# Kernel optimization log

Measured on AMD Instinct MI355X. Metric: run time of the kernel, lower is better.

The kernel has to match this reference:

```python
import jax, jax.numpy as jnp
import numpy as np
from jax import lax

ALPHA = 100.0      # SuperSpike surrogate slope (LIFParameters alpha)
DT = 1e-3          # norse default dt
TAU_SYN_INV = 200.0
TAU_MEM_INV = 100.0
V_TH = 1.0

@jax.custom_vjp
def superspike(x):
    return (x > 0).astype(x.dtype)

def _ss_fwd(x):
    return (x > 0).astype(x.dtype), x

def _ss_bwd(x, g):
    return (g / (ALPHA * jnp.abs(x) + 1.0) ** 2,)

superspike.defvjp(_ss_fwd, _ss_bwd)

def lif_step(inp, v, i):
    # norse lif_step: decay v/i, spike on v_decayed - v_th, reset, then add input current
    v_dec = v + DT * TAU_MEM_INV * (-v + i)
    i_dec = i * (1.0 - DT * TAU_SYN_INV)
    z = superspike(v_dec - V_TH)
    v_new = (1.0 - z) * v_dec  # v_reset = 0
    i_new = i_dec + inp
    return z, v_new, i_new

def li_step(inp, v, i):
    # leaky integrator readout (LILinearCell): returns membrane voltage
    v_new = v + DT * TAU_MEM_INV * (-v + i)
    i_new = i * (1.0 - DT * TAU_SYN_INV) + inp
    return v_new, v_new, i_new

def conv2d(x, w, b):
    y = lax.conv_general_dilated(x, w, (1, 1), 'VALID',
                                 dimension_numbers=('NCHW', 'OIHW', 'NCHW'))
    return y + b[None, :, None, None]

def maxpool2(x):
    return lax.reduce_window(x, -jnp.inf, lax.max, (1, 1, 2, 2), (1, 1, 2, 2), 'VALID')

def setup_inputs() -> dict:
    key = jax.random.key(0)
    ks = jax.random.split(key, 9)
    T, B, C, H = 16, 64, 3, 64
    feats = int(((H - 4) / 2 - 4) / 2)  # 13
    def unif(k, shape, fan_in):
        bound = 1.0 / np.sqrt(fan_in)
        return jax.random.uniform(k, shape, jnp.float32, -bound, bound)
    return {
        'x':  jax.random.normal(ks[0], (T, B, C, H, H), jnp.float32),
        'w1': unif(ks[1], (32, C, 5, 5), C * 25),
        'b1': unif(ks[2], (32,), C * 25),
        'w2': unif(ks[3], (64, 32, 5, 5), 32 * 25),
        'b2': unif(ks[4], (64,), 32 * 25),
        'wf': unif(ks[5], (1024, feats * feats * 64), feats * feats * 64),
        'bf': unif(ks[6], (1024,), feats * feats * 64),
        'wo': unif(ks[7], (10, 1024), 1024),
        'bo': unif(ks[8], (10,), 1024),
    }

def reference(x, w1, b1, w2, b2, wf, bf, wo, bo):
    T, B, C, H, _ = x.shape
    h1 = H - 4           # conv1 out spatial
    p1 = h1 // 2         # pool1
    h2 = p1 - 4          # conv2 out spatial
    p2 = h2 // 2         # pool2 (== features)
    dtype = x.dtype
    zeros = lambda s: jnp.zeros(s, dtype)
    carry0 = (zeros((B, 32, h1, h1)), zeros((B, 32, h1, h1)),   # lif0 v, i
              zeros((B, 64, h2, h2)), zeros((B, 64, h2, h2)),   # lif1 v, i
              zeros((B, 1024)), zeros((B, 1024)),               # lif2 v, i
              zeros((B, 10)), zeros((B, 10)))                   # out  v, i

    def step(carry, xt):
        v0, i0, v1, i1, v2, i2, vo, io = carry
        z = conv2d(xt, w1, b1)
        z, v0, i0 = lif_step(z, v0, i0)
        z = maxpool2(z)
        z = 10.0 * conv2d(z, w2, b2)
        z, v1, i1 = lif_step(z, v1, i1)
        z = maxpool2(z)
        z = z.reshape(B, -1)
        z = z @ wf.T + bf
        z, v2, i2 = lif_step(z, v2, i2)
        inp = jax.nn.relu(z) @ wo.T + bo
        v, vo, io = li_step(inp, vo, io)
        return (v0, i0, v1, i1, v2, i2, vo, io), v

    _, voltages = lax.scan(step, carry0, x)
    return voltages  # [T, B, 10]
```

## Files before the change

### kernel.cpp

```cpp
#include <hip/hip_runtime.h>

typedef __attribute__((ext_vector_type(8))) short short8v;
typedef __attribute__((ext_vector_type(4))) float f32x4;

#define DT_TM 0.1f
#define SYN_DEC 0.8f
#define TT 16
#define BB 64
#define FCK 10816

#define BO_S1   ((size_t)0)
#define BO_S2   ((size_t)29491200)
#define BO_S3   ((size_t)51642368)
#define BO_PART ((size_t)55836672)
#define BO_WH2  BO_PART
#define BO_WL2  (BO_PART + 102400)
#define BO_AFW  (BO_PART + 204800)
#define BO_WHF  ((size_t)72613888)
#define BO_WLF  ((size_t)94765056)
#define BIG_NEED ((size_t)116916224)

#define FO_S1   ((size_t)0)
#define FO_S2   ((size_t)29491200)
#define FO_S3   ((size_t)40566784)
#define FO_PART ((size_t)44761088)
#define FO_V2   ((size_t)51576832)
#define FO_I2   ((size_t)51838976)
#define FO_WH2  FO_PART
#define FO_WL2  (FO_PART + 102400)

__device__ __forceinline__ unsigned short bf16_rne(float f) {
  unsigned int u = __float_as_uint(f);
  return (unsigned short)((u + 0x7FFFu + ((u >> 16) & 1u)) >> 16);
}

__global__ __launch_bounds__(256) void k0_prep(
    const float* __restrict__ w2, unsigned short* __restrict__ whi,
    unsigned short* __restrict__ wlo) {
  int e = blockIdx.x * 256 + threadIdx.x;
  if (e >= 25 * 64 * 32) return;
  int kk = e >> 11;
  int rem = e & 2047;
  int oc = rem >> 5, c = rem & 31;
  float w = w2[(size_t)(oc * 32 + c) * 25 + kk];
  unsigned short hi = bf16_rne(w);
  float fhi = __uint_as_float((unsigned int)hi << 16);
  unsigned short lo = bf16_rne(w - fhi);
  whi[e] = hi;
  wlo[e] = lo;
}

__global__ __launch_bounds__(256) void k0b_wf(
    const float* __restrict__ wf, unsigned short* __restrict__ whiF,
    unsigned short* __restrict__ wloF) {
  size_t e = (size_t)blockIdx.x * 256 + threadIdx.x;
  if (e >= (size_t)1024 * FCK) return;
  float w = wf[e];
  unsigned short hi = bf16_rne(w);
  float fhi = __uint_as_float((unsigned int)hi << 16);
  whiF[e] = hi;
  wloF[e] = bf16_rne(w - fhi);
}

__global__ __launch_bounds__(256) void k0w_prep(
    const float* __restrict__ w1, unsigned short* __restrict__ afw) {
  int e = blockIdx.x * 256 + threadIdx.x;
  if (e >= 9216) return;
  int i = e & 7, l = (e >> 3) & 63, f = e >> 9;
  int sp = f % 3, ks = (f / 3) % 3, mt = f / 9;
  int oc = mt * 16 + (l & 15);
  int tap = (l >> 4) * 8 + i;
  unsigned short out = 0;
  int ky = tap / 6, kx = tap - 6 * ky;
  if (tap < 30 && kx < 5) {
    float v = w1[(oc * 3 + ks) * 25 + ky * 5 + kx];
    unsigned short h = bf16_rne(v);
    if (sp == 0) out = h;
    else {
      float r1 = v - __uint_as_float((unsigned int)h << 16);
      unsigned short m = bf16_rne(r1);
      if (sp == 1) out = m;
      else out = bf16_rne(r1 - __uint_as_float((unsigned int)m << 16));
    }
  }
  afw[e] = out;
}

#define MFMA_BF16 __builtin_amdgcn_mfma_f32_16x16x32_bf16

__global__ __launch_bounds__(256) void k1_mfma(
    const float* __restrict__ x, const unsigned short* __restrict__ afw,
    const float* __restrict__ b1, unsigned char* __restrict__ s1) {
  __shared__ unsigned int Hp[2][18 * 81];
  __shared__ unsigned int Mp[2][18 * 81];
  __shared__ unsigned int Lp[2][18 * 81];
  const int s = blockIdx.x;
  const int b = blockIdx.y;
  const int tid = threadIdx.x;
  const int w = tid >> 6, l = tid & 63;
  const int n = l & 15, tg = l >> 4;
  const int xpix = 16 * w + n;
  const int xcl = (xpix < 60) ? xpix : 59;
  const bool storer = ((n & 1) == 0) && (xpix < 60);

  short8v aw[2][3][3];
#pragma unroll
  for (int mt = 0; mt < 2; ++mt)
#pragma unroll
    for (int ks = 0; ks < 3; ++ks)
#pragma unroll
      for (int sp = 0; sp < 3; ++sp)
        aw[mt][ks][sp] =
            *(const short8v*)(afw + (((mt * 3 + ks) * 3 + sp) * 64 + l) * 8);

  f32x4 bias0 = *(const f32x4*)&b1[tg * 4];
  f32x4 bias1 = *(const f32x4*)&b1[16 + tg * 4];

  int poff[4];
#pragma unroll
  for (int i = 0; i < 4; ++i) {
    int tap = tg * 8 + 2 * i;
    int ky = tap / 6, kx = tap - 6 * ky;
    if (tap >= 30) { ky = 4; kx = 0; }
    poff[i] = ky * 81 + kx;
  }

  const int jrow0 = tid >> 5, jcp0 = tid & 31;
  const int jrow1 = (tid + 256) >> 5, jcp1 = jcp0;
  const int jrow2 = (tid + 512) >> 5, jcp2 = jcp0;
  const bool job2 = tid < 64;
  const int slan = (l & 32) | ((l + 1) & 31);

  float vst[2][2][4], ist[2][2][4];
#pragma unroll
  for (int a = 0; a < 2; ++a)
#pragma unroll
    for (int m = 0; m < 2; ++m)
#pragma unroll
      for (int r = 0; r < 4; ++r) { vst[a][m][r] = 0.f; ist[a][m][r] = 0.f; }

  float2 pf0, pf1, pf2;

  auto phaseA = [&](int t) {
    const float* xp = x + ((size_t)(t * BB + b)) * 12288 + (size_t)(2 * s) * 64;
    {
      int c = jrow0 / 6, r = jrow0 - 6 * c;
      pf0 = *(const float2*)(xp + c * 4096 + r * 64 + 2 * jcp0);
    }
    {
      int c = jrow1 / 6, r = jrow1 - 6 * c;
      pf1 = *(const float2*)(xp + c * 4096 + r * 64 + 2 * jcp1);
    }
    if (job2) {
      int c = jrow2 / 6, r = jrow2 - 6 * c;
      pf2 = *(const float2*)(xp + c * 4096 + r * 64 + 2 * jcp2);
    }
  };

  auto phaseB = [&](int bfi) {
    unsigned int* H = Hp[bfi];
    unsigned int* M = Mp[bfi];
    unsigned int* L = Lp[bfi];
#pragma unroll
    for (int j = 0; j < 3; ++j) {
      if (j == 2 && !job2) break;
      float2 v2 = (j == 0) ? pf0 : (j == 1) ? pf1 : pf2;
      int row = (j == 0) ? jrow0 : (j == 1) ? jrow1 : jrow2;
      int cp = jcp0;
      unsigned int h0 = bf16_rne(v2.x);
      float r0 = v2.x - __uint_as_float(h0 << 16);
      unsigned int m0 = bf16_rne(r0);
      unsigned int l0 = bf16_rne(r0 - __uint_as_float(m0 << 16));
      unsigned int h1 = bf16_rne(v2.y);
      float r1 = v2.y - __uint_as_float(h1 << 16);
      unsigned int m1 = bf16_rne(r1);
      unsigned int l1 = bf16_rne(r1 - __uint_as_float(m1 << 16));
      unsigned int hm0 = h0 | (m0 << 16);
      unsigned int hmN = (unsigned int)__shfl((int)hm0, slan);
      unsigned int lN  = (unsigned int)__shfl((int)l0, slan);
      int d = row * 81 + 2 * cp;
      H[d]     = h0 | (h1 << 16);
      H[d + 1] = h1 | (hmN << 16);
      M[d]     = m0 | (m1 << 16);
      M[d + 1] = m1 | (hmN & 0xffff0000u);
      L[d]     = l0 | (l1 << 16);
      L[d + 1] = l1 | (lN << 16);
    }
  };

  phaseA(0);
  phaseB(0);
  __syncthreads();

  for (int t = 0; t < TT; ++t) {
    const int cur = t & 1;
    if (t + 1 < TT) phaseA(t + 1);

    const unsigned int* H = Hp[cur];
    const unsigned int* M = Mp[cur];
    const unsigned int* L = Lp[cur];

    unsigned int pk[2];
#pragma unroll
    for (int nt = 0; nt < 2; ++nt) {
      f32x4 acc0 = (f32x4){0.f, 0.f, 0.f, 0.f};
      f32x4 acc1 = (f32x4){0.f, 0.f, 0.f, 0.f};
#pragma unroll
      for (int ks = 0; ks < 3; ++ks) {
        const int base = (ks * 6 + nt) * 81 + xcl;
        union { unsigned int u[4]; short8v v; } fH, fM, fL;
#pragma unroll
        for (int i = 0; i < 4; ++i) {
          fH.u[i] = H[base + poff[i]];
          fM.u[i] = M[base + poff[i]];
          fL.u[i] = L[base + poff[i]];
        }
        acc0 = MFMA_BF16(aw[0][ks][2], fH.v, acc0, 0, 0, 0);
        acc1 = MFMA_BF16(aw[1][ks][2], fH.v, acc1, 0, 0, 0);
        acc0 = MFMA_BF16(aw[0][ks][1], fM.v, acc0, 0, 0, 0);
        acc1 = MFMA_BF16(aw[1][ks][1], fM.v, acc1, 0, 0, 0);
        acc0 = MFMA_BF16(aw[0][ks][0], fL.v, acc0, 0, 0, 0);
        acc1 = MFMA_BF16(aw[1][ks][0], fL.v, acc1, 0, 0, 0);
        acc0 = MFMA_BF16(aw[0][ks][1], fH.v, acc0, 0, 0, 0);
        acc1 = MFMA_BF16(aw[1][ks][1], fH.v, acc1, 0, 0, 0);
        acc0 = MFMA_BF16(aw[0][ks][0], fM.v, acc0, 0, 0, 0);
        acc1 = MFMA_BF16(aw[1][ks][0], fM.v, acc1, 0, 0, 0);
        acc0 = MFMA_BF16(aw[0][ks][0], fH.v, acc0, 0, 0, 0);
        acc1 = MFMA_BF16(aw[1][ks][0], fH.v, acc1, 0, 0, 0);
      }
      unsigned int nib0 = 0, nib1 = 0;
#pragma unroll
      for (int r = 0; r < 4; ++r) {
        float inp = acc0[r] + bias0[r];
        float vd = vst[nt][0][r] + DT_TM * (ist[nt][0][r] - vst[nt][0][r]);
        float id = SYN_DEC * ist[nt][0][r];
        bool z = vd > 1.0f;
        vst[nt][0][r] = z ? 0.f : vd;
        ist[nt][0][r] = id + inp;
// ... 37 lines not shown
  const int tid = threadIdx.x;
  const bool valid = tid < 225;
  const int py0 = (tid / 15) * 2;
  const int px0 = (tid % 15) * 2;
  const int br = 2 * py0;
  const int bc = 2 * px0;

  float v[16], cur[16];
#pragma unroll
  for (int j = 0; j < 16; ++j) { v[j] = 0.f; cur[j] = 0.f; }
  const float bias = b1[oc];

  for (int t = 0; t < TT; ++t) {
    const float* xp = x + ((size_t)(t * BB + b)) * 12288;
#pragma unroll
    for (int k = 0; k < 12; ++k) {
      int e = tid + k * 256;
      int row = e >> 4, c4 = e & 15;
      ((float4*)xs)[row * 17 + c4] = ((const float4*)xp)[e];
    }
    __syncthreads();

    if (valid) {
      float acc[4][4];
#pragma unroll
      for (int r = 0; r < 4; ++r)
#pragma unroll
        for (int s = 0; s < 4; ++s) acc[r][s] = 0.f;

#pragma unroll
      for (int c = 0; c < 3; ++c) {
        const float* wp = w1 + (oc * 3 + c) * 25;
        float wv[25];
#pragma unroll
        for (int j = 0; j < 25; ++j) wv[j] = wp[j];
#pragma unroll
        for (int ri = 0; ri < 8; ++ri) {
          const float* rowp = &xs[(c * 64 + br + ri) * 68 + bc];
          float4 ra = *(const float4*)rowp;
          float4 rb = *(const float4*)(rowp + 4);
          float row[8] = {ra.x, ra.y, ra.z, ra.w, rb.x, rb.y, rb.z, rb.w};
#pragma unroll
          for (int r = 0; r < 4; ++r) {
            int ky = ri - r;
            if (ky >= 0 && ky < 5) {
#pragma unroll
              for (int kx = 0; kx < 5; ++kx) {
                float w = wv[ky * 5 + kx];
#pragma unroll
                for (int s = 0; s < 4; ++s) acc[r][s] += w * row[s + kx];
              }
            }
          }
        }
      }

      unsigned char pz00 = 0, pz01 = 0, pz10 = 0, pz11 = 0;
#pragma unroll
      for (int r = 0; r < 4; ++r)
#pragma unroll
        for (int s = 0; s < 4; ++s) {
          int j = r * 4 + s;
          float vd = v[j] + DT_TM * (cur[j] - v[j]);
          float id = SYN_DEC * cur[j];
          float inp = acc[r][s] + bias;
          bool z = vd > 1.0f;
          v[j] = z ? 0.f : vd;
          cur[j] = id + inp;
          if (z) {
            if (r < 2) { if (s < 2) pz00 = 1; else pz01 = 1; }
            else       { if (s < 2) pz10 = 1; else pz11 = 1; }
          }
        }
      size_t pixb = ((size_t)(t * BB + b)) * 900;
      s1[(pixb + (size_t)py0 * 30 + px0) * 32 + oc]           = pz00;
      s1[(pixb + (size_t)py0 * 30 + px0 + 1) * 32 + oc]       = pz01;
      s1[(pixb + (size_t)(py0 + 1) * 30 + px0) * 32 + oc]     = pz10;
      s1[(pixb + (size_t)(py0 + 1) * 30 + px0 + 1) * 32 + oc] = pz11;
    }
    __syncthreads();
  }
}

template<int NT>
__device__ __forceinline__ void k2_wave(
    const unsigned short* sl, float* Vst, float* Ist, unsigned char* zbuf,
    const unsigned short* __restrict__ whi, const unsigned short* __restrict__ wlo,
    const float* __restrict__ b2, int og, int q, int n, int ntstart, int npos) {
  int baddr[NT], pcl[NT];
  f32x4 acc[2][NT];
#pragma unroll
  for (int j = 0; j < NT; ++j) {
    int pl = (ntstart + j) * 16 + n;
    if (pl > npos - 1) pl = npos - 1;
    pcl[j] = pl;
    int ry = pl / 26, xx = pl - ry * 26;
    baddr[j] = (ry * 30 + xx) * 32 + q * 8;
    acc[0][j] = (f32x4){0.f, 0.f, 0.f, 0.f};
    acc[1][j] = (f32x4){0.f, 0.f, 0.f, 0.f};
  }
  const int abase = (og * 32 + n) * 32 + q * 8;
#pragma unroll 5
  for (int kk = 0; kk < 25; ++kk) {
    const int ky = kk / 5, kx = kk - (kk / 5) * 5;
    const int off = (ky * 30 + kx) * 32;
    short8v ah0 = *(const short8v*)(whi + kk * 2048 + abase);
    short8v al0 = *(const short8v*)(wlo + kk * 2048 + abase);
    short8v ah1 = *(const short8v*)(whi + kk * 2048 + abase + 512);
    short8v al1 = *(const short8v*)(wlo + kk * 2048 + abase + 512);
#pragma unroll
    for (int j = 0; j < NT; ++j) {
      short8v bv = *(const short8v*)(sl + baddr[j] + off);
      acc[0][j] = MFMA_BF16(al0, bv, acc[0][j], 0, 0, 0);
      acc[0][j] = MFMA_BF16(ah0, bv, acc[0][j], 0, 0, 0);
      acc[1][j] = MFMA_BF16(al1, bv, acc[1][j], 0, 0, 0);
      acc[1][j] = MFMA_BF16(ah1, bv, acc[1][j], 0, 0, 0);
    }
  }
  const f32x4 bias0 = *(const f32x4*)&b2[og * 32 + q * 4];
  const f32x4 bias1 = *(const f32x4*)&b2[og * 32 + 16 + q * 4];
#pragma unroll
  for (int j = 0; j < NT; ++j) {
    int p = pcl[j];
#pragma unroll
    for (int mi = 0; mi < 2; ++mi) {
      int sidx = p * 68 + og * 32 + mi * 16 + q * 4;
      f32x4 v4 = *(f32x4*)&Vst[sidx];
      f32x4 i4 = *(f32x4*)&Ist[sidx];
      f32x4 bia = mi ? bias1 : bias0;
      f32x4 a = acc[mi][j];
      unsigned char zr[4];
#pragma unroll
      for (int r = 0; r < 4; ++r) {
        float vd = v4[r] + DT_TM * (i4[r] - v4[r]);
        float id = SYN_DEC * i4[r];
        float inp = 10.f * (a[r] + bia[r]);
        bool z = vd > 1.0f;
        v4[r] = z ? 0.f : vd;
        i4[r] = id + inp;
        zr[r] = z ? 1 : 0;
      }
      *(f32x4*)&Vst[sidx] = v4;
      *(f32x4*)&Ist[sidx] = i4;
      *(uchar4*)&zbuf[sidx] = make_uchar4(zr[0], zr[1], zr[2], zr[3]);
    }
  }
}

template<typename ST>
__global__ __launch_bounds__(256) void k2_mfma(
    const unsigned char* __restrict__ s1, const unsigned short* __restrict__ whi,
    const unsigned short* __restrict__ wlo, const float* __restrict__ b2,
    ST* __restrict__ s2) {
  __shared__ unsigned short sl[12 * 30 * 32];
  __shared__ float Vst[208 * 68];
  __shared__ float Ist[208 * 68];
  __shared__ unsigned char zbuf[208 * 68];
  const int quad = blockIdx.x, b = blockIdx.y;
  const int tid = threadIdx.x;
  const int wid = tid >> 6, l = tid & 63;
  const int og = wid & 1, nc = wid >> 1;
  const int q = l >> 4, n = l & 15;
  const int y0 = (quad == 0) ? 0 : (2 + quad * 6);
  const int R  = (quad == 0) ? 8 : 6;
  const int inRows = R + 4;
  const int npos = R * 26;

  for (int e = tid; e < 208 * 68; e += 256) { Vst[e] = 0.f; Ist[e] = 0.f; }
  __syncthreads();

  for (int t = 0; t < TT; ++t) {
    const unsigned char* sp =
        s1 + (((size_t)(t * BB + b)) * 900 + (size_t)y0 * 30) * 32;
    const int nelem = inRows * 240;
    for (int e = tid; e < nelem; e += 256) {
      unsigned int w = *(const unsigned int*)(sp + (size_t)e * 4);
      unsigned int lo = ((w & 0xFFu) ? 0x3F80u : 0u) |
                        ((w & 0xFF00u) ? 0x3F800000u : 0u);
      unsigned int hi = ((w & 0xFF0000u) ? 0x3F80u : 0u) |
                        ((w & 0xFF000000u) ? 0x3F800000u : 0u);
      ((unsigned int*)sl)[e * 2]     = lo;
      ((unsigned int*)sl)[e * 2 + 1] = hi;
    }
    __syncthreads();

    if (quad == 0) {
      if (nc == 0) k2_wave<7>(sl, Vst, Ist, zbuf, whi, wlo, b2, og, q, n, 0, npos);
      else         k2_wave<6>(sl, Vst, Ist, zbuf, whi, wlo, b2, og, q, n, 7, npos);
    } else {
      k2_wave<5>(sl, Vst, Ist, zbuf, whi, wlo, b2, og, q, n, nc * 5, npos);
    }
    __syncthreads();

    const int pr = R >> 1;
    const int pcount = pr * 13 * 64;
    ST* s2p = s2 + ((size_t)(t * BB + b)) * 64 * 169;
    const int gpy0 = y0 >> 1;
    const ST one = (ST)((sizeof(ST) == 2) ? 0x3F80 : 1);
    for (int e = tid; e < pcount; e += 256) {
      int oc = e & 63, pp = e >> 6;
      int ppy = pp / 13, ppx = pp - ppy * 13;
      int base = (2 * ppy * 26 + 2 * ppx) * 68 + oc;
      unsigned char z = (unsigned char)(zbuf[base] | zbuf[base + 68] |
                        zbuf[base + 26 * 68] | zbuf[base + 26 * 68 + 68]);
      s2p[(size_t)oc * 169 + (gpy0 + ppy) * 13 + ppx] = z ? one : (ST)0;
    }
    __syncthreads();
  }
}

__global__ __launch_bounds__(512) void k3g_fc(
    const unsigned short* __restrict__ s2,
    const unsigned short* __restrict__ whiF,
    const unsigned short* __restrict__ wloF,
    float* __restrict__ part) {
  __shared__ __align__(16) unsigned short As[128][72];
  __shared__ __align__(16) unsigned short Bh[128][72];
  __shared__ __align__(16) unsigned short Bl[128][72];
  const int tid = threadIdx.x;
  const int w = tid >> 6, l = tid & 63;
  const int mh = w & 1, nq = w >> 1;
  const int lr = l & 15, lk = l >> 4;
  const int n0 = blockIdx.x * 128, m0 = blockIdx.y * 128;
  const int ks = blockIdx.z;
  const int s_begin = (169 * ks) >> 2, s_end = (169 * (ks + 1)) >> 2;

  const int arow = tid >> 2, aseg = tid & 3;
  const unsigned short* ap = s2 + (size_t)(m0 + arow) * FCK + aseg * 16;
  unsigned short* aq = &As[0][0] + arow * 72 + aseg * 16;
  const int barr = tid >> 8, brem = tid & 255;
  const int bn = brem >> 1, bhalf = brem & 1;
  const unsigned short* bp =
      (barr ? wloF : whiF) + (size_t)(n0 + bn) * FCK + bhalf * 32;
  unsigned short* bq = (barr ? &Bl[0][0] : &Bh[0][0]) + bn * 72 + bhalf * 32;

  f32x4 acc[4][2];
#pragma unroll
  for (int mt = 0; mt < 4; ++mt)
#pragma unroll
    for (int nt = 0; nt < 2; ++nt) acc[mt][nt] = (f32x4){0.f, 0.f, 0.f, 0.f};

  for (int s = s_begin; s < s_end; ++s) {
    const size_t k0 = (size_t)s * 64;
    short8v a0 = *(const short8v*)(ap + k0);
    short8v a1 = *(const short8v*)(ap + k0 + 8);
    short8v b0 = *(const short8v*)(bp + k0);
    short8v b1 = *(const short8v*)(bp + k0 + 8);
    short8v b2v = *(const short8v*)(bp + k0 + 16);
    short8v b3 = *(const short8v*)(bp + k0 + 24);
    __syncthreads();
    *(short8v*)(aq)      = a0;
    *(short8v*)(aq + 8)  = a1;
    *(short8v*)(bq)      = b0;
    *(short8v*)(bq + 8)  = b1;
    *(short8v*)(bq + 16) = b2v;
    *(short8v*)(bq + 24) = b3;
    __syncthreads();
#pragma unroll
    for (int kt = 0; kt < 2; ++kt) {
      short8v bh0 = *(const short8v*)&Bh[nq * 32 + lr][kt * 32 + lk * 8];
      short8v bh1 = *(const short8v*)&Bh[nq * 32 + 16 + lr][kt * 32 + lk * 8];
      short8v bl0 = *(const short8v*)&Bl[nq * 32 + lr][kt * 32 + lk * 8];
      short8v bl1 = *(const short8v*)&Bl[nq * 32 + 16 + lr][kt * 32 + lk * 8];
#pragma unroll
      for (int mt = 0; mt < 4; ++mt) {
        short8v af = *(const short8v*)&As[mh * 64 + mt * 16 + lr][kt * 32 + lk * 8];
        acc[mt][0] = MFMA_BF16(af, bh0, acc[mt][0], 0, 0, 0);
        acc[mt][0] = MFMA_BF16(af, bl0, acc[mt][0], 0, 0, 0);
        acc[mt][1] = MFMA_BF16(af, bh1, acc[mt][1], 0, 0, 0);
        acc[mt][1] = MFMA_BF16(af, bl1, acc[mt][1], 0, 0, 0);
      }
    }
  }
  float* pp = part + ((size_t)ks << 20);
#pragma unroll
  for (int mt = 0; mt < 4; ++mt)
#pragma unroll
    for (int nt = 0; nt < 2; ++nt) {
      int mrow = m0 + mh * 64 + mt * 16 + lk * 4;
      int ncol = n0 + nq * 32 + nt * 16 + lr;
#pragma unroll
      for (int r = 0; r < 4; ++r)
        pp[(size_t)(mrow + r) * 1024 + ncol] = acc[mt][nt][r];
    }
}

__global__ __launch_bounds__(256) void k3r_lif2(
    const float* __restrict__ part, const float* __restrict__ bf,
    float* __restrict__ s3) {
  int e = blockIdx.x * 256 + threadIdx.x;
// ... 57 lines not shown
      float a0 = av.x, a1 = av.y, a2 = av.z, a3 = av.w;
      acc[0][0] += a0 * bv.x; acc[0][1] += a0 * bv.y; acc[0][2] += a0 * bv.z; acc[0][3] += a0 * bv.w;
      acc[1][0] += a1 * bv.x; acc[1][1] += a1 * bv.y; acc[1][2] += a1 * bv.z; acc[1][3] += a1 * bv.w;
      acc[2][0] += a2 * bv.x; acc[2][1] += a2 * bv.y; acc[2][2] += a2 * bv.z; acc[2][3] += a2 * bv.w;
      acc[3][0] += a3 * bv.x; acc[3][1] += a3 * bv.y; acc[3][2] += a3 * bv.z; acc[3][3] += a3 * bv.w;
    }
  }
#pragma unroll
  for (int i = 0; i < 4; ++i)
#pragma unroll
    for (int j = 0; j < 4; ++j)
      part[((size_t)(ks * 64 + m0 + i)) * 1024 + N0 + n0 + j] = acc[i][j];
}

__global__ __launch_bounds__(256) void k3b_lif2(
    const float* __restrict__ part, const float* __restrict__ bf,
    float* __restrict__ v2, float* __restrict__ i2,
    float* __restrict__ s3, int t) {
  int e = blockIdx.x * 256 + threadIdx.x;
  int n = e & 1023;
  float s = 0.f;
#pragma unroll
  for (int ks = 0; ks < 26; ++ks) s += part[(size_t)ks * 65536 + e];
  float z = s + bf[n];
  float vv = v2[e], ii = i2[e];
  float vd = vv + DT_TM * (ii - vv);
  float id = SYN_DEC * ii;
  bool sp = vd > 1.0f;
  v2[e] = sp ? 0.f : vd;
  i2[e] = id + z;
  s3[(size_t)t * 65536 + e] = sp ? 1.f : 0.f;
}

__global__ __launch_bounds__(320) void k4_out(
    const float* __restrict__ s3, const float* __restrict__ wo,
    const float* __restrict__ bo, float* __restrict__ out) {
  const int b = blockIdx.x;
  const int g = threadIdx.x >> 5;
  const int l = threadIdx.x & 31;
  float vv = 0.f, ii = 0.f;
  const float bg = bo[g];
  for (int t = 0; t < TT; ++t) {
    const float* zp = s3 + ((size_t)t * BB + b) * 1024;
    const float* wp = wo + g * 1024;
    float p = 0.f;
#pragma unroll 8
    for (int j = l; j < 1024; j += 32) p += zp[j] * wp[j];
#pragma unroll
    for (int off = 16; off; off >>= 1) p += __shfl_down(p, off, 32);
    float inp = p + bg;
    float vn = vv + DT_TM * (ii - vv);
    if (l == 0) out[(size_t)(t * BB + b) * 10 + g] = vn;
    ii = SYN_DEC * ii + inp;
    vv = vn;
  }
}

extern "C" void kernel_launch(void* const* d_in, const int* in_sizes, int n_in,
                              void* d_out, int out_size, void* d_ws, size_t ws_size,
                              hipStream_t stream) {
  (void)in_sizes; (void)n_in; (void)out_size;
  const float* x  = (const float*)d_in[0];
  const float* w1 = (const float*)d_in[1];
  const float* b1 = (const float*)d_in[2];
  const float* w2 = (const float*)d_in[3];
  const float* b2 = (const float*)d_in[4];
  const float* wf = (const float*)d_in[5];
  const float* bf = (const float*)d_in[6];
  const float* wo = (const float*)d_in[7];
  const float* bo = (const float*)d_in[8];
  float* out = (float*)d_out;
  char* ws = (char*)d_ws;

  if (ws_size >= BIG_NEED) {
    unsigned char*  s1   = (unsigned char*)(ws + BO_S1);
    unsigned short* s2   = (unsigned short*)(ws + BO_S2);
    float*          s3   = (float*)(ws + BO_S3);
    float*          part = (float*)(ws + BO_PART);
    unsigned short* wh2  = (unsigned short*)(ws + BO_WH2);
    unsigned short* wl2  = (unsigned short*)(ws + BO_WL2);
    unsigned short* afw  = (unsigned short*)(ws + BO_AFW);
    unsigned short* whiF = (unsigned short*)(ws + BO_WHF);
    unsigned short* wloF = (unsigned short*)(ws + BO_WLF);

    k0_prep<<<dim3(200), 256, 0, stream>>>(w2, wh2, wl2);
    k0w_prep<<<dim3(36), 256, 0, stream>>>(w1, afw);
    k0b_wf<<<dim3(43264), 256, 0, stream>>>(wf, whiF, wloF);
    k1_mfma<<<dim3(30, 64), 256, 0, stream>>>(x, afw, b1, s1);
    k2_mfma<unsigned short><<<dim3(4, 64), 256, 0, stream>>>(s1, wh2, wl2, b2, s2);
    k3g_fc<<<dim3(8, 8, 4), 512, 0, stream>>>(s2, whiF, wloF, part);
    k3r_lif2<<<dim3(256), 256, 0, stream>>>(part, bf, s3);
    k4_out<<<dim3(64), 320, 0, stream>>>(s3, wo, bo, out);
  } else {
    unsigned char*  s1   = (unsigned char*)(ws + FO_S1);
    unsigned char*  s2   = (unsigned char*)(ws + FO_S2);
    float*          s3   = (float*)(ws + FO_S3);
    float*          part = (float*)(ws + FO_PART);
    float*          v2   = (float*)(ws + FO_V2);
    float*          i2   = (float*)(ws + FO_I2);
    unsigned short* wh2  = (unsigned short*)(ws + FO_WH2);
    unsigned short* wl2  = (unsigned short*)(ws + FO_WL2);

    hipMemsetAsync(v2, 0, 2 * 65536 * sizeof(float), stream);
    k0_prep<<<dim3(200), 256, 0, stream>>>(w2, wh2, wl2);
    k1_conv1<<<dim3(32, 64), 256, 0, stream>>>(x, w1, b1, s1);
    k2_mfma<unsigned char><<<dim3(4, 64), 256, 0, stream>>>(s1, wh2, wl2, b2, s2);
    for (int t = 0; t < TT; ++t) {
      k3a_fc<<<dim3(16, 26), 256, 0, stream>>>(s2, wf, part, t);
      k3b_lif2<<<dim3(256), 256, 0, stream>>>(part, bf, v2, i2, s3, t);
    }
    k4_out<<<dim3(64), 320, 0, stream>>>(s3, wo, bo, out);
  }
}
```

Measured before the change: 517.6 us.

## Keep conv2 LIF membrane state in registers instead of shared memory

The conv2 kernel's per-wave work is restructured so each wave owns its output tile for all timesteps and keeps the LIF voltage and current state in registers across the time loop. This removes the large Vst/Ist shared-memory arrays (about 113 KB) and their per-step loads and stores, which should allow two blocks per CU, now requested via launch_bounds(256,2). The kk loop unroll is reduced from 5 to 2 to limit register pressure. The risk is register spilling from the extra state arrays, which can reach 112 floats per thread for NT=7.

Result: slower. 709.2 us (+37.0%).

```diff
diff --git a/kernel.cpp b/kernel.cpp
--- a/kernel.cpp
+++ b/kernel.cpp
@@ -126,8 +126,8 @@
   }
 
   const int jrow0 = tid >> 5, jcp0 = tid & 31;
-  const int jrow1 = (tid + 256) >> 5, jcp1 = jcp0;
-  const int jrow2 = (tid + 512) >> 5, jcp2 = jcp0;
+  const int jrow1 = (tid + 256) >> 5;
+  const int jrow2 = (tid + 512) >> 5;
   const bool job2 = tid < 64;
   const int slan = (l & 32) | ((l + 1) & 31);
 
@@ -149,11 +149,11 @@
     }
     {
       int c = jrow1 / 6, r = jrow1 - 6 * c;
-      pf1 = *(const float2*)(xp + c * 4096 + r * 64 + 2 * jcp1);
+      pf1 = *(const float2*)(xp + c * 4096 + r * 64 + 2 * jcp0);
     }
     if (job2) {
       int c = jrow2 / 6, r = jrow2 - 6 * c;
-      pf2 = *(const float2*)(xp + c * 4096 + r * 64 + 2 * jcp2);
+      pf2 = *(const float2*)(xp + c * 4096 + r * 64 + 2 * jcp0);
     }
   };
 
@@ -357,13 +357,15 @@
   }
 }
 
-template<int NT>
-__device__ __forceinline__ void k2_wave(
-    const unsigned short* sl, float* Vst, float* Ist, unsigned char* zbuf,
-    const unsigned short* __restrict__ whi, const unsigned short* __restrict__ wlo,
-    const float* __restrict__ b2, int og, int q, int n, int ntstart, int npos) {
+template<int NT, typename ST>
+__device__ __forceinline__ void k2_run(
+    const unsigned char* __restrict__ s1, const unsigned short* __restrict__ whi,
+    const unsigned short* __restrict__ wlo, const float* __restrict__ b2,
+    ST* __restrict__ s2, unsigned short* sl, unsigned char* zbuf,
+    int b, int og, int q, int n, int ntstart, int npos, int y0, int R) {
+  const int tid = threadIdx.x;
+  const int inRows = R + 4;
   int baddr[NT], pcl[NT];
-  f32x4 acc[2][NT];
 #pragma unroll
   for (int j = 0; j < NT; ++j) {
     int pl = (ntstart + j) * 16 + n;
@@ -371,78 +373,18 @@
     pcl[j] = pl;
     int ry = pl / 26, xx = pl - ry * 26;
     baddr[j] = (ry * 30 + xx) * 32 + q * 8;
-    acc[0][j] = (f32x4){0.f, 0.f, 0.f, 0.f};
-    acc[1][j] = (f32x4){0.f, 0.f, 0.f, 0.f};
   }
   const int abase = (og * 32 + n) * 32 + q * 8;
-#pragma unroll 5
-  for (int kk = 0; kk < 25; ++kk) {
-    const int ky = kk / 5, kx = kk - (kk / 5) * 5;
-    const int off = (ky * 30 + kx) * 32;
-    short8v ah0 = *(const short8v*)(whi + kk * 2048 + abase);
-    short8v al0 = *(const short8v*)(wlo + kk * 2048 + abase);
-    short8v ah1 = *(const short8v*)(whi + kk * 2048 + abase + 512);
-    short8v al1 = *(const short8v*)(wlo + kk * 2048 + abase + 512);
-#pragma unroll
-    for (int j = 0; j < NT; ++j) {
-      short8v bv = *(const short8v*)(sl + baddr[j] + off);
-      acc[0][j] = MFMA_BF16(al0, bv, acc[0][j], 0, 0, 0);
-      acc[0][j] = MFMA_BF16(ah0, bv, acc[0][j], 0, 0, 0);
-      acc[1][j] = MFMA_BF16(al1, bv, acc[1][j], 0, 0, 0);
-      acc[1][j] = MFMA_BF16(ah1, bv, acc[1][j], 0, 0, 0);
-    }
-  }
   const f32x4 bias0 = *(const f32x4*)&b2[og * 32 + q * 4];
   const f32x4 bias1 = *(const f32x4*)&b2[og * 32 + 16 + q * 4];
-#pragma unroll
-  for (int j = 0; j < NT; ++j) {
-    int p = pcl[j];
-#pragma unroll
-    for (int mi = 0; mi < 2; ++mi) {
-      int sidx = p * 68 + og * 32 + mi * 16 + q * 4;
-      f32x4 v4 = *(f32x4*)&Vst[sidx];
-      f32x4 i4 = *(f32x4*)&Ist[sidx];
-      f32x4 bia = mi ? bias1 : bias0;
-      f32x4 a = acc[mi][j];
-      unsigned char zr[4];
-#pragma unroll
-      for (int r = 0; r < 4; ++r) {
-        float vd = v4[r] + DT_TM * (i4[r] - v4[r]);
-        float id = SYN_DEC * i4[r];
-        float inp = 10.f * (a[r] + bia[r]);
-        bool z = vd > 1.0f;
-        v4[r] = z ? 0.f : vd;
-        i4[r] = id + inp;
-        zr[r] = z ? 1 : 0;
-      }
-      *(f32x4*)&Vst[sidx] = v4;
-      *(f32x4*)&Ist[sidx] = i4;
-      *(uchar4*)&zbuf[sidx] = make_uchar4(zr[0], zr[1], zr[2], zr[3]);
-    }
-  }
-}
-
-template<typename ST>
-__global__ __launch_bounds__(256) void k2_mfma(
-    const unsigned char* __restrict__ s1, const unsigned short* __restrict__ whi,
-    const unsigned short* __restrict__ wlo, const float* __restrict__ b2,
-    ST* __restrict__ s2) {
-  __shared__ unsigned short sl[12 * 30 * 32];
-  __shared__ float Vst[208 * 68];
-  __shared__ float Ist[208 * 68];
-  __shared__ unsigned char zbuf[208 * 68];
-  const int quad = blockIdx.x, b = blockIdx.y;
-  const int tid = threadIdx.x;
-  const int wid = tid >> 6, l = tid & 63;
-  const int og = wid & 1, nc = wid >> 1;
-  const int q = l >> 4, n = l & 15;
-  const int y0 = (quad == 0) ? 0 : (2 + quad * 6);
-  const int R  = (quad == 0) ? 8 : 6;
-  const int inRows = R + 4;
-  const int npos = R * 26;
-
-  for (int e = tid; e < 208 * 68; e += 256) { Vst[e] = 0.f; Ist[e] = 0.f; }
-  __syncthreads();
+
+  float vst[2][NT][4], ist[2][NT][4];
+#pragma unroll
+  for (int mi = 0; mi < 2; ++mi)
+#pragma unroll
+    for (int j = 0; j < NT; ++j)
+#pragma unroll
+      for (int r = 0; r < 4; ++r) { vst[mi][j][r] = 0.f; ist[mi][j][r] = 0.f; }
 
   for (int t = 0; t < TT; ++t) {
     const unsigned char* sp =
@@ -459,16 +401,57 @@
     }
     __syncthreads();
 
-    if (quad == 0) {
-      if (nc == 0) k2_wave<7>(sl, Vst, Ist, zbuf, whi, wlo, b2, og, q, n, 0, npos);
-      else         k2_wave<6>(sl, Vst, Ist, zbuf, whi, wlo, b2, og, q, n, 7, npos);
-    } else {
-      k2_wave<5>(sl, Vst, Ist, zbuf, whi, wlo, b2, og, q, n, nc * 5, npos);
-    }
-    __syncthreads();
-
-    const int pr = R >> 1;
-    const int pcount = pr * 13 * 64;
+    f32x4 acc[2][NT];
+#pragma unroll
+    for (int mi = 0; mi < 2; ++mi)
+#pragma unroll
+      for (int j = 0; j < NT; ++j) acc[mi][j] = (f32x4){0.f, 0.f, 0.f, 0.f};
+
+#pragma unroll 2
+    for (int kk = 0; kk < 25; ++kk) {
+      const int ky = kk / 5, kx = kk - (kk / 5) * 5;
+      const int off = (ky * 30 + kx) * 32;
+      short8v ah0 = *(const short8v*)(whi + kk * 2048 + abase);
+      short8v al0 = *(const short8v*)(wlo + kk * 2048 + abase);
+      short8v ah1 = *(const short8v*)(whi + kk * 2048 + abase + 512);
+      short8v al1 = *(const short8v*)(wlo + kk * 2048 + abase + 512);
+#pragma unroll
+      for (int j = 0; j < NT; ++j) {
+        short8v bv = *(const short8v*)(sl + baddr[j] + off);
+        acc[0][j] = MFMA_BF16(al0, bv, acc[0][j], 0, 0, 0);
+        acc[0][j] = MFMA_BF16(ah0, bv, acc[0][j], 0, 0, 0);
+        acc[1][j] = MFMA_BF16(al1, bv, acc[1][j], 0, 0, 0);
+        acc[1][j] = MFMA_BF16(ah1, bv, acc[1][j], 0, 0, 0);
+      }
+    }
+
+#pragma unroll
+    for (int j = 0; j < NT; ++j) {
+      int p = pcl[j];
+#pragma unroll
+      for (int mi = 0; mi < 2; ++mi) {
+        int sidx = p * 68 + og * 32 + mi * 16 + q * 4;
+        f32x4 bia = mi ? bias1 : bias0;
+        f32x4 a = acc[mi][j];
+        unsigned char zr[4];
+#pragma unroll
+        for (int r = 0; r < 4; ++r) {
+          float vv = vst[mi][j][r], ii = ist[mi][j][r];
+          float vd = vv + DT_TM * (ii - vv);
+          float id = SYN_DEC * ii;
+          float inp = 10.f * (a[r] + bia[r]);
+          bool z = vd > 1.0f;
+          vst[mi][j][r] = z ? 0.f : vd;
+          ist[mi][j][r] = id + inp;
+          zr[r] = z ? 1 : 0;
+        }
+        *(uchar4*)&zbuf[sidx] = make_uchar4(zr[0], zr[1], zr[2], zr[3]);
+      }
+    }
+    __syncthreads();
+
+    const int prr = R >> 1;
+    const int pcount = prr * 13 * 64;
     ST* s2p = s2 + ((size_t)(t * BB + b)) * 64 * 169;
     const int gpy0 = y0 >> 1;
     const ST one = (ST)((sizeof(ST) == 2) ? 0x3F80 : 1);
@@ -481,6 +464,32 @@
       s2p[(size_t)oc * 169 + (gpy0 + ppy) * 13 + ppx] = z ? one : (ST)0;
     }
     __syncthreads();
+  }
+}
+
+template<typename ST>
+__global__ __launch_bounds__(256, 2) void k2_mfma(
+    const unsigned char* __restrict__ s1, const unsigned short* __restrict__ whi,
+    const unsigned short* __restrict__ wlo, const float* __restrict__ b2,
+    ST* __restrict__ s2) {
+  __shared__ unsigned short sl[12 * 30 * 32];
+  __shared__ unsigned char zbuf[208 * 68];
+  const int quad = blockIdx.x, b = blockIdx.y;
+  const int tid = threadIdx.x;
+  const int wid = tid >> 6, l = tid & 63;
+  const int og = wid & 1, nc = wid >> 1;
+  const int q = l >> 4, n = l & 15;
+  const int y0 = (quad == 0) ? 0 : (2 + quad * 6);
+  const int R  = (quad == 0) ? 8 : 6;
+  const int npos = R * 26;
+
+  if (quad == 0) {
+    if (nc == 0)
+      k2_run<7, ST>(s1, whi, wlo, b2, s2, sl, zbuf, b, og, q, n, 0, npos, y0, R);
+    else
+      k2_run<6, ST>(s1, whi, wlo, b2, s2, sl, zbuf, b, og, q, n, 7, npos, y0, R);
+  } else {
+    k2_run<5, ST>(s1, whi, wlo, b2, s2, sl, zbuf, b, og, q, n, nc * 5, npos, y0, R);
   }
 }
 
```

## Move conv2 LIF state from LDS to global workspace to raise occupancy

Applied to the files above, without the earlier changes.

Adds a k2 variant that keeps the per-block LIF membrane and current state in a global workspace buffer instead of two large shared-memory arrays. This cuts LDS use per block (about 113KB down to about 37KB), so more blocks or waves can be resident. The cost is extra global reads and writes of state every timestep, which should mostly hit cache. The variant is used only when the workspace is large enough, otherwise the old LDS kernel runs.

After: 664.0 us. +28.3%, slower.

```diff
diff --git a/kernel.cpp b/kernel.cpp
--- a/kernel.cpp
+++ b/kernel.cpp
@@ -19,6 +19,9 @@
 #define BO_WHF  ((size_t)72613888)
 #define BO_WLF  ((size_t)94765056)
 #define BIG_NEED ((size_t)116916224)
+#define BO_KST  BIG_NEED
+#define KST_SZ  ((size_t)27262976)
+#define BIG2_NEED (BO_KST + KST_SZ)
 
 #define FO_S1   ((size_t)0)
 #define FO_S2   ((size_t)29491200)
@@ -126,8 +129,8 @@
   }
 
   const int jrow0 = tid >> 5, jcp0 = tid & 31;
-  const int jrow1 = (tid + 256) >> 5, jcp1 = jcp0;
-  const int jrow2 = (tid + 512) >> 5, jcp2 = jcp0;
+  const int jrow1 = (tid + 256) >> 5;
+  const int jrow2 = (tid + 512) >> 5;
   const bool job2 = tid < 64;
   const int slan = (l & 32) | ((l + 1) & 31);
 
@@ -149,11 +152,11 @@
     }
     {
       int c = jrow1 / 6, r = jrow1 - 6 * c;
-      pf1 = *(const float2*)(xp + c * 4096 + r * 64 + 2 * jcp1);
+      pf1 = *(const float2*)(xp + c * 4096 + r * 64 + 2 * jcp0);
     }
     if (job2) {
       int c = jrow2 / 6, r = jrow2 - 6 * c;
-      pf2 = *(const float2*)(xp + c * 4096 + r * 64 + 2 * jcp2);
+      pf2 = *(const float2*)(xp + c * 4096 + r * 64 + 2 * jcp0);
     }
   };
 
@@ -357,6 +360,153 @@
   }
 }
 
+template<typename ST>
+__device__ __forceinline__ void k2_stage(
+    const unsigned char* __restrict__ s1, unsigned short* sl,
+    int t, int b, int y0, int inRows) {
+  const int tid = threadIdx.x;
+  const unsigned char* sp =
+      s1 + (((size_t)(t * BB + b)) * 900 + (size_t)y0 * 30) * 32;
+  const int nelem = inRows * 240;
+  for (int e = tid; e < nelem; e += 256) {
+    unsigned int w = *(const unsigned int*)(sp + (size_t)e * 4);
+    unsigned int lo = ((w & 0xFFu) ? 0x3F80u : 0u) |
+                      ((w & 0xFF00u) ? 0x3F800000u : 0u);
+    unsigned int hi = ((w & 0xFF0000u) ? 0x3F80u : 0u) |
+                      ((w & 0xFF000000u) ? 0x3F800000u : 0u);
+    ((unsigned int*)sl)[e * 2]     = lo;
+    ((unsigned int*)sl)[e * 2 + 1] = hi;
+  }
+}
+
+template<typename ST>
+__device__ __forceinline__ void k2_pool(
+    ST* __restrict__ s2, const unsigned char* zbuf, int t, int b, int y0, int R) {
+  const int tid = threadIdx.x;
+  const int prr = R >> 1;
+  const int pcount = prr * 13 * 64;
+  ST* s2p = s2 + ((size_t)(t * BB + b)) * 64 * 169;
+  const int gpy0 = y0 >> 1;
+  const ST one = (ST)((sizeof(ST) == 2) ? 0x3F80 : 1);
+  for (int e = tid; e < pcount; e += 256) {
+    int oc = e & 63, pp = e >> 6;
+    int ppy = pp / 13, ppx = pp - ppy * 13;
+    int base = (2 * ppy * 26 + 2 * ppx) * 68 + oc;
+    unsigned char z = (unsigned char)(zbuf[base] | zbuf[base + 68] |
+                      zbuf[base + 26 * 68] | zbuf[base + 26 * 68 + 68]);
+    s2p[(size_t)oc * 169 + (gpy0 + ppy) * 13 + ppx] = z ? one : (ST)0;
+  }
+}
+
+template<int NT>
+__device__ __forceinline__ void k2g_wave(
+    const unsigned short* sl, float* __restrict__ kstb, unsigned char* zbuf,
+    const unsigned short* __restrict__ whi, const unsigned short* __restrict__ wlo,
+    const float* __restrict__ b2, int og, int q, int n, int ntstart, int npos,
+    bool first) {
+  int baddr[NT], pcl[NT];
+  f32x4 acc[2][NT];
+#pragma unroll
+  for (int j = 0; j < NT; ++j) {
+    int pl = (ntstart + j) * 16 + n;
+    if (pl > npos - 1) pl = npos - 1;
+    pcl[j] = pl;
+    int ry = pl / 26, xx = pl - ry * 26;
+    baddr[j] = (ry * 30 + xx) * 32 + q * 8;
+    acc[0][j] = (f32x4){0.f, 0.f, 0.f, 0.f};
+    acc[1][j] = (f32x4){0.f, 0.f, 0.f, 0.f};
+  }
+  const int abase = (og * 32 + n) * 32 + q * 8;
+#pragma unroll 5
+  for (int kk = 0; kk < 25; ++kk) {
+    const int ky = kk / 5, kx = kk - (kk / 5) * 5;
+    const int off = (ky * 30 + kx) * 32;
+    short8v ah0 = *(const short8v*)(whi + kk * 2048 + abase);
+    short8v al0 = *(const short8v*)(wlo + kk * 2048 + abase);
+    short8v ah1 = *(const short8v*)(whi + kk * 2048 + abase + 512);
+    short8v al1 = *(const short8v*)(wlo + kk * 2048 + abase + 512);
+#pragma unroll
+    for (int j = 0; j < NT; ++j) {
+      short8v bv = *(const short8v*)(sl + baddr[j] + off);
+      acc[0][j] = MFMA_BF16(al0, bv, acc[0][j], 0, 0, 0);
+      acc[0][j] = MFMA_BF16(ah0, bv, acc[0][j], 0, 0, 0);
+      acc[1][j] = MFMA_BF16(al1, bv, acc[1][j], 0, 0, 0);
+      acc[1][j] = MFMA_BF16(ah1, bv, acc[1][j], 0, 0, 0);
+    }
+  }
+  const f32x4 bias0 = *(const f32x4*)&b2[og * 32 + q * 4];
+  const f32x4 bias1 = *(const f32x4*)&b2[og * 32 + 16 + q * 4];
+#pragma unroll
+  for (int j = 0; j < NT; ++j) {
+    int p = pcl[j];
+#pragma unroll
+    for (int mi = 0; mi < 2; ++mi) {
+      const int zidx = p * 68 + og * 32 + mi * 16 + q * 4;
+      float* gp = kstb + (size_t)p * 128 + og * 32 + mi * 16 + q * 4;
+      f32x4 v4, i4;
+      if (first) {
+        v4 = (f32x4){0.f, 0.f, 0.f, 0.f};
+        i4 = (f32x4){0.f, 0.f, 0.f, 0.f};
+      } else {
+        v4 = *(const f32x4*)gp;
+        i4 = *(const f32x4*)(gp + 64);
+      }
+      f32x4 bia = mi ? bias1 : bias0;
+      f32x4 a = acc[mi][j];
+      unsigned char zr[4];
+#pragma unroll
+      for (int r = 0; r < 4; ++r) {
+        float vd = v4[r] + DT_TM * (i4[r] - v4[r]);
+        float id = SYN_DEC * i4[r];
+        float inp = 10.f * (a[r] + bia[r]);
+        bool z = vd > 1.0f;
+        v4[r] = z ? 0.f : vd;
+        i4[r] = id + inp;
+        zr[r] = z ? 1 : 0;
+      }
+      *(f32x4*)gp = v4;
+      *(f32x4*)(gp + 64) = i4;
+      *(uchar4*)&zbuf[zidx] = make_uchar4(zr[0], zr[1], zr[2], zr[3]);
+    }
+  }
+}
+
+template<typename ST>
+__global__ __launch_bounds__(256) void k2_mfma_g(
+    const unsigned char* __restrict__ s1, const unsigned short* __restrict__ whi,
+    const unsigned short* __restrict__ wlo, const float* __restrict__ b2,
+    ST* __restrict__ s2, float* __restrict__ kst) {
+  __shared__ unsigned short sl[12 * 30 * 32];
+  __shared__ unsigned char zbuf[208 * 68];
+  const int quad = blockIdx.x, b = blockIdx.y;
+  const int tid = threadIdx.x;
+  const int wid = tid >> 6, l = tid & 63;
+  const int og = wid & 1, nc = wid >> 1;
+  const int q = l >> 4, n = l & 15;
+  const int y0 = (quad == 0) ? 0 : (2 + quad * 6);
+  const int R  = (quad == 0) ? 8 : 6;
+  const int inRows = R + 4;
+  const int npos = R * 26;
+  float* kstb = kst + (size_t)(quad * 64 + b) * 208 * 128;
+
+  for (int t = 0; t < TT; ++t) {
+    k2_stage<ST>(s1, sl, t, b, y0, inRows);
+    __syncthreads();
+
+    const bool first = (t == 0);
+    if (quad == 0) {
+      if (nc == 0) k2g_wave<7>(sl, kstb, zbuf, whi, wlo, b2, og, q, n, 0, npos, first);
+      else         k2g_wave<6>(sl, kstb, zbuf, whi, wlo, b2, og, q, n, 7, npos, first);
+    } else {
+      k2g_wave<5>(sl, kstb, zbuf, whi, wlo, b2, og, q, n, nc * 5, npos, first);
+    }
+    __syncthreads();
+
+    k2_pool<ST>(s2, zbuf, t, b, y0, R);
+    __syncthreads();
+  }
+}
+
 template<int NT>
 __device__ __forceinline__ void k2_wave(
     const unsigned short* sl, float* Vst, float* Ist, unsigned char* zbuf,
@@ -423,7 +573,7 @@
 }
 
 template<typename ST>
-__global__ __launch_bounds__(256) void k2_mfma(
+__global__ __launch_bounds__(256) void k2_mfma_l(
     const unsigned char* __restrict__ s1, const unsigned short* __restrict__ whi,
     const unsigned short* __restrict__ wlo, const float* __restrict__ b2,
     ST* __restrict__ s2) {
@@ -445,18 +595,7 @@
   __syncthreads();
 
   for (int t = 0; t < TT; ++t) {
-    const unsigned char* sp =
-        s1 + (((size_t)(t * BB + b)) * 900 + (size_t)y0 * 30) * 32;
-    const int nelem = inRows * 240;
-    for (int e = tid; e < nelem; e += 256) {
-      unsigned int w = *(const unsigned int*)(sp + (size_t)e * 4);
-      unsigned int lo = ((w & 0xFFu) ? 0x3F80u : 0u) |
-                        ((w & 0xFF00u) ? 0x3F800000u : 0u);
-      unsigned int hi = ((w & 0xFF0000u) ? 0x3F80u : 0u) |
-                        ((w & 0xFF000000u) ? 0x3F800000u : 0u);
-      ((unsigned int*)sl)[e * 2]     = lo;
-      ((unsigned int*)sl)[e * 2 + 1] = hi;
-    }
+    k2_stage<ST>(s1, sl, t, b, y0, inRows);
     __syncthreads();
 
     if (quad == 0) {
@@ -467,19 +606,7 @@
     }
     __syncthreads();
 
-    const int pr = R >> 1;
-    const int pcount = pr * 13 * 64;
-    ST* s2p = s2 + ((size_t)(t * BB + b)) * 64 * 169;
-    const int gpy0 = y0 >> 1;
-    const ST one = (ST)((sizeof(ST) == 2) ? 0x3F80 : 1);
-    for (int e = tid; e < pcount; e += 256) {
-      int oc = e & 63, pp = e >> 6;
-      int ppy = pp / 13, ppx = pp - ppy * 13;
-      int base = (2 * ppy * 26 + 2 * ppx) * 68 + oc;
-      unsigned char z = (unsigned char)(zbuf[base] | zbuf[base + 68] |
-                        zbuf[base + 26 * 68] | zbuf[base + 26 * 68 + 68]);
-      s2p[(size_t)oc * 169 + (gpy0 + ppy) * 13 + ppx] = z ? one : (ST)0;
-    }
+    k2_pool<ST>(s2, zbuf, t, b, y0, R);
     __syncthreads();
   }
 }
@@ -704,12 +831,18 @@
     unsigned short* afw  = (unsigned short*)(ws + BO_AFW);
     unsigned short* whiF = (unsigned short*)(ws + BO_WHF);
     unsigned short* wloF = (unsigned short*)(ws + BO_WLF);
+    float*          kst  = (float*)(ws + BO_KST);
 
     k0_prep<<<dim3(200), 256, 0, stream>>>(w2, wh2, wl2);
     k0w_prep<<<dim3(36), 256, 0, stream>>>(w1, afw);
     k0b_wf<<<dim3(43264), 256, 0, stream>>>(wf, whiF, wloF);
     k1_mfma<<<dim3(30, 64), 256, 0, stream>>>(x, afw, b1, s1);
-    k2_mfma<unsigned short><<<dim3(4, 64), 256, 0, stream>>>(s1, wh2, wl2, b2, s2);
+    if (ws_size >= BIG2_NEED)
+      k2_mfma_g<unsigned short><<<dim3(4, 64), 256, 0, stream>>>(
+          s1, wh2, wl2, b2, s2, kst);
+    else
+      k2_mfma_l<unsigned short><<<dim3(4, 64), 256, 0, stream>>>(
+          s1, wh2, wl2, b2, s2);
     k3g_fc<<<dim3(8, 8, 4), 512, 0, stream>>>(s2, whiF, wloF, part);
     k3r_lif2<<<dim3(256), 256, 0, stream>>>(part, bf, s3);
     k4_out<<<dim3(64), 320, 0, stream>>>(s3, wo, bo, out);
@@ -726,7 +859,7 @@
     hipMemsetAsync(v2, 0, 2 * 65536 * sizeof(float), stream);
     k0_prep<<<dim3(200), 256, 0, stream>>>(w2, wh2, wl2);
     k1_conv1<<<dim3(32, 64), 256, 0, stream>>>(x, w1, b1, s1);
-    k2_mfma<unsigned char><<<dim3(4, 64), 256, 0, stream>>>(s1, wh2, wl2, b2, s2);
+    k2_mfma_l<unsigned char><<<dim3(4, 64), 256, 0, stream>>>(s1, wh2, wl2, b2, s2);
     for (int t = 0; t < TT; ++t) {
       k3a_fc<<<dim3(16, 26), 256, 0, stream>>>(s2, wf, part, t);
       k3b_lif2<<<dim3(256), 256, 0, stream>>>(part, bf, v2, i2, s3, t);
```

## Prefetch next timestep's spike tile and double-buffer conv2 MFMA operands

Applied to the files above, without the earlier changes.

In the conv2 kernel, the global load of the next timestep's spike input is issued into registers before the current step's MFMA work. It is written to shared memory after pooling, which removes one barrier and the exposed global load latency per step. The inner 25-tap MFMA loop is fully unrolled with register double-buffering, so weights and shared-memory operands for tap k+1 are loaded while tap k computes. This costs more registers (12 prefetch words plus duplicated operand sets), which may lower occupancy or cause spills.

Result: slower. 631.6 us (+22.0%).

```diff
diff --git a/kernel.cpp b/kernel.cpp
--- a/kernel.cpp
+++ b/kernel.cpp
@@ -126,8 +126,8 @@
   }
 
   const int jrow0 = tid >> 5, jcp0 = tid & 31;
-  const int jrow1 = (tid + 256) >> 5, jcp1 = jcp0;
-  const int jrow2 = (tid + 512) >> 5, jcp2 = jcp0;
+  const int jrow1 = (tid + 256) >> 5;
+  const int jrow2 = (tid + 512) >> 5;
   const bool job2 = tid < 64;
   const int slan = (l & 32) | ((l + 1) & 31);
 
@@ -149,11 +149,11 @@
     }
     {
       int c = jrow1 / 6, r = jrow1 - 6 * c;
-      pf1 = *(const float2*)(xp + c * 4096 + r * 64 + 2 * jcp1);
+      pf1 = *(const float2*)(xp + c * 4096 + r * 64 + 2 * jcp0);
     }
     if (job2) {
       int c = jrow2 / 6, r = jrow2 - 6 * c;
-      pf2 = *(const float2*)(xp + c * 4096 + r * 64 + 2 * jcp2);
+      pf2 = *(const float2*)(xp + c * 4096 + r * 64 + 2 * jcp0);
     }
   };
 
@@ -357,6 +357,58 @@
   }
 }
 
+__device__ __forceinline__ void k2_stage_load(
+    const unsigned char* __restrict__ s1, unsigned int (&pf)[12],
+    int t, int b, int y0, int inRows) {
+  const int tid = threadIdx.x;
+  const unsigned char* sp =
+      s1 + (((size_t)(t * BB + b)) * 900 + (size_t)y0 * 30) * 32;
+  const int nelem = inRows * 240;
+#pragma unroll
+  for (int i = 0; i < 12; ++i) {
+    int e = tid + i * 256;
+    if (e < nelem) pf[i] = *(const unsigned int*)(sp + (size_t)e * 4);
+  }
+}
+
+__device__ __forceinline__ void k2_stage_write(
+    unsigned short* sl, const unsigned int (&pf)[12], int inRows) {
+  const int tid = threadIdx.x;
+  const int nelem = inRows * 240;
+#pragma unroll
+  for (int i = 0; i < 12; ++i) {
+    int e = tid + i * 256;
+    if (e < nelem) {
+      unsigned int w = pf[i];
+      unsigned int lo = ((w & 0xFFu) ? 0x3F80u : 0u) |
+                        ((w & 0xFF00u) ? 0x3F800000u : 0u);
+      unsigned int hi = ((w & 0xFF0000u) ? 0x3F80u : 0u) |
+                        ((w & 0xFF000000u) ? 0x3F800000u : 0u);
+      ((unsigned int*)sl)[e * 2]     = lo;
+      ((unsigned int*)sl)[e * 2 + 1] = hi;
+    }
+  }
+}
+
+template<typename ST>
+__device__ __forceinline__ void k2_pool(
+    ST* __restrict__ s2, const unsigned char* zbuf, int t, int b, int y0, int R) {
+  const int tid = threadIdx.x;
+  const int prr = R >> 1;
+  const int pcount = prr * 13 * 64;
+  ST* s2p = s2 + ((size_t)(t * BB + b)) * 64 * 169;
+  const int gpy0 = y0 >> 1;
+  const ST one = (ST)((sizeof(ST) == 2) ? 0x3F80 : 1);
+  for (int e = tid; e < pcount; e += 256) {
+    int oc = e & 63, pp = e >> 6;
+    int ppy = pp / 13, ppx = pp - ppy * 13;
+    int base = (2 * ppy * 26 + 2 * ppx) * 68 + oc;
+    unsigned char z = (unsigned char)(zbuf[base] | zbuf[base + 68] |
+                      zbuf[base + 26 * 68] | zbuf[base + 26 * 68 + 68]);
+    s2p[(size_t)oc * 169 + (gpy0 + ppy) * 13 + ppx] = z ? one : (ST)0;
+  }
+}
+
 template<int NT>
 __device__ __forceinline__ void k2_wave(
     const unsigned short* sl, float* Vst, float* Ist, unsigned char* zbuf,
@@ -375,23 +427,47 @@
     acc[1][j] = (f32x4){0.f, 0.f, 0.f, 0.f};
   }
   const int abase = (og * 32 + n) * 32 + q * 8;
-#pragma unroll 5
+  const unsigned short* whik = whi + abase;
+  const unsigned short* wlok = wlo + abase;
+
+  short8v ah0c = *(const short8v*)(whik);
+  short8v al0c = *(const short8v*)(wlok);
+  short8v ah1c = *(const short8v*)(whik + 512);
+  short8v al1c = *(const short8v*)(wlok + 512);
+  short8v bc[NT];
+#pragma unroll
+  for (int j = 0; j < NT; ++j) bc[j] = *(const short8v*)(sl + baddr[j]);
+
+#pragma unroll
   for (int kk = 0; kk < 25; ++kk) {
-    const int ky = kk / 5, kx = kk - (kk / 5) * 5;
-    const int off = (ky * 30 + kx) * 32;
-    short8v ah0 = *(const short8v*)(whi + kk * 2048 + abase);
-    short8v al0 = *(const short8v*)(wlo + kk * 2048 + abase);
-    short8v ah1 = *(const short8v*)(whi + kk * 2048 + abase + 512);
-    short8v al1 = *(const short8v*)(wlo + kk * 2048 + abase + 512);
+    short8v ah0n, al0n, ah1n, al1n;
+    short8v bn[NT];
+    if (kk < 24) {
+      const int kn = kk + 1;
+      const int kyn = kn / 5, kxn = kn - 5 * (kn / 5);
+      const int offn = (kyn * 30 + kxn) * 32;
+      ah0n = *(const short8v*)(whik + kn * 2048);
+      al0n = *(const short8v*)(wlok + kn * 2048);
+      ah1n = *(const short8v*)(whik + kn * 2048 + 512);
+      al1n = *(const short8v*)(wlok + kn * 2048 + 512);
+#pragma unroll
+      for (int j = 0; j < NT; ++j)
+        bn[j] = *(const short8v*)(sl + baddr[j] + offn);
+    }
 #pragma unroll
     for (int j = 0; j < NT; ++j) {
-      short8v bv = *(const short8v*)(sl + baddr[j] + off);
-      acc[0][j] = MFMA_BF16(al0, bv, acc[0][j], 0, 0, 0);
-      acc[0][j] = MFMA_BF16(ah0, bv, acc[0][j], 0, 0, 0);
-      acc[1][j] = MFMA_BF16(al1, bv, acc[1][j], 0, 0, 0);
-      acc[1][j] = MFMA_BF16(ah1, bv, acc[1][j], 0, 0, 0);
-    }
-  }
+      acc[0][j] = MFMA_BF16(al0c, bc[j], acc[0][j], 0, 0, 0);
+      acc[0][j] = MFMA_BF16(ah0c, bc[j], acc[0][j], 0, 0, 0);
+      acc[1][j] = MFMA_BF16(al1c, bc[j], acc[1][j], 0, 0, 0);
+      acc[1][j] = MFMA_BF16(ah1c, bc[j], acc[1][j], 0, 0, 0);
+    }
+    if (kk < 24) {
+      ah0c = ah0n; al0c = al0n; ah1c = ah1n; al1c = al1n;
+#pragma unroll
+      for (int j = 0; j < NT; ++j) bc[j] = bn[j];
+    }
+  }
+
   const f32x4 bias0 = *(const f32x4*)&b2[og * 32 + q * 4];
   const f32x4 bias1 = *(const f32x4*)&b2[og * 32 + 16 + q * 4];
 #pragma unroll
@@ -423,7 +499,7 @@
 }
 
 template<typename ST>
-__global__ __launch_bounds__(256) void k2_mfma(
+__global__ __launch_bounds__(256) void k2_mfma_l(
     const unsigned char* __restrict__ s1, const unsigned short* __restrict__ whi,
     const unsigned short* __restrict__ wlo, const float* __restrict__ b2,
     ST* __restrict__ s2) {
@@ -442,22 +518,14 @@
   const int npos = R * 26;
 
   for (int e = tid; e < 208 * 68; e += 256) { Vst[e] = 0.f; Ist[e] = 0.f; }
+
+  unsigned int pf[12];
+  k2_stage_load(s1, pf, 0, b, y0, inRows);
+  k2_stage_write(sl, pf, inRows);
   __syncthreads();
 
   for (int t = 0; t < TT; ++t) {
-    const unsigned char* sp =
-        s1 + (((size_t)(t * BB + b)) * 900 + (size_t)y0 * 30) * 32;
-    const int nelem = inRows * 240;
-    for (int e = tid; e < nelem; e += 256) {
-      unsigned int w = *(const unsigned int*)(sp + (size_t)e * 4);
-      unsigned int lo = ((w & 0xFFu) ? 0x3F80u : 0u) |
-                        ((w & 0xFF00u) ? 0x3F800000u : 0u);
-      unsigned int hi = ((w & 0xFF0000u) ? 0x3F80u : 0u) |
-                        ((w & 0xFF000000u) ? 0x3F800000u : 0u);
-      ((unsigned int*)sl)[e * 2]     = lo;
-      ((unsigned int*)sl)[e * 2 + 1] = hi;
-    }
-    __syncthreads();
+    if (t + 1 < TT) k2_stage_load(s1, pf, t + 1, b, y0, inRows);
 
     if (quad == 0) {
       if (nc == 0) k2_wave<7>(sl, Vst, Ist, zbuf, whi, wlo, b2, og, q, n, 0, npos);
@@ -467,19 +535,8 @@
     }
     __syncthreads();
 
-    const int pr = R >> 1;
-    const int pcount = pr * 13 * 64;
-    ST* s2p = s2 + ((size_t)(t * BB + b)) * 64 * 169;
-    const int gpy0 = y0 >> 1;
-    const ST one = (ST)((sizeof(ST) == 2) ? 0x3F80 : 1);
-    for (int e = tid; e < pcount; e += 256) {
-      int oc = e & 63, pp = e >> 6;
-      int ppy = pp / 13, ppx = pp - ppy * 13;
-      int base = (2 * ppy * 26 + 2 * ppx) * 68 + oc;
-      unsigned char z = (unsigned char)(zbuf[base] | zbuf[base + 68] |
-                        zbuf[base + 26 * 68] | zbuf[base + 26 * 68 + 68]);
-      s2p[(size_t)oc * 169 + (gpy0 + ppy) * 13 + ppx] = z ? one : (ST)0;
-    }
+    k2_pool<ST>(s2, zbuf, t, b, y0, R);
+    if (t + 1 < TT) k2_stage_write(sl, pf, inRows);
     __syncthreads();
   }
 }
@@ -709,7 +766,8 @@
     k0w_prep<<<dim3(36), 256, 0, stream>>>(w1, afw);
     k0b_wf<<<dim3(43264), 256, 0, stream>>>(wf, whiF, wloF);
     k1_mfma<<<dim3(30, 64), 256, 0, stream>>>(x, afw, b1, s1);
-    k2_mfma<unsigned short><<<dim3(4, 64), 256, 0, stream>>>(s1, wh2, wl2, b2, s2);
+    k2_mfma_l<unsigned short><<<dim3(4, 64), 256, 0, stream>>>(
+        s1, wh2, wl2, b2, s2);
     k3g_fc<<<dim3(8, 8, 4), 512, 0, stream>>>(s2, whiF, wloF, part);
     k3r_lif2<<<dim3(256), 256, 0, stream>>>(part, bf, s3);
     k4_out<<<dim3(64), 320, 0, stream>>>(s3, wo, bo, out);
@@ -726,7 +784,7 @@
     hipMemsetAsync(v2, 0, 2 * 65536 * sizeof(float), stream);
     k0_prep<<<dim3(200), 256, 0, stream>>>(w2, wh2, wl2);
     k1_conv1<<<dim3(32, 64), 256, 0, stream>>>(x, w1, b1, s1);
-    k2_mfma<unsigned char><<<dim3(4, 64), 256, 0, stream>>>(s1, wh2, wl2, b2, s2);
+    k2_mfma_l<unsigned char><<<dim3(4, 64), 256, 0, stream>>>(s1, wh2, wl2, b2, s2);
     for (int t = 0; t < TT; ++t) {
       k3a_fc<<<dim3(16, 26), 256, 0, stream>>>(s2, wf, part, t);
       k3b_lif2<<<dim3(256), 256, 0, stream>>>(part, bf, v2, i2, s3, t);
```
